# Optimization experiments

Measured on AMD Instinct MI355X. Metric: run time of the kernel, lower is better.

## Reference

```python
import jax, jax.numpy as jnp
import numpy as np

WS = 8            # window size (square)
NUM_HEADS = 8
DIM = 256
IMG = 256         # feature map H=W for mask construction
SHIFT = WS // 2
B = 4


def _rel_pos_index(Wh, Ww):
    coords = np.stack(np.meshgrid(np.arange(Wh), np.arange(Ww), indexing='ij'))  # (2,Wh,Ww)
    cf = coords.reshape(2, -1)
    rel = cf[:, :, None] - cf[:, None, :]        # (2,N,N)
    rel = rel.transpose(1, 2, 0).astype(np.int64)
    rel[..., 0] += Wh - 1
    rel[..., 1] += Ww - 1
    rel[..., 0] *= 2 * Ww - 1
    return rel.sum(-1)                           # (N,N)


def _shift_mask(H, W, ws, ss):
    # standard Swin shifted-window attention mask: (nW, ws*ws, ws*ws) with 0 / -100
    img = np.zeros((H, W), dtype=np.float32)
    cnt = 0
    for hs in (slice(0, -ws), slice(-ws, -ss), slice(-ss, None)):
        for wsl in (slice(0, -ws), slice(-ws, -ss), slice(-ss, None)):
            img[hs, wsl] = cnt
            cnt += 1
    m = img.reshape(H // ws, ws, W // ws, ws).transpose(0, 2, 1, 3).reshape(-1, ws * ws)
    am = m[:, None, :] - m[:, :, None]
    return np.where(am != 0, np.float32(-100.0), np.float32(0.0))


def setup_inputs() -> dict:
    key = jax.random.key(0)
    ks = jax.random.split(key, 10)
    nW = (IMG // WS) ** 2
    B_ = B * nW
    N = WS * WS
    x = jax.random.normal(ks[0], (B_, N, DIM), dtype=jnp.float32)
    y = jax.random.normal(ks[1], (B_, N, DIM), dtype=jnp.float32)
    mask = jnp.asarray(_shift_mask(IMG, IMG, WS, SHIFT))
    s = 0.02
    q_w = jax.random.normal(ks[2], (DIM, DIM), dtype=jnp.float32) * s
    q_b = jnp.zeros((DIM,), dtype=jnp.float32)
    kv_w = jax.random.normal(ks[3], (2 * DIM, DIM), dtype=jnp.float32) * s
    kv_b = jnp.zeros((2 * DIM,), dtype=jnp.float32)
    proj_w = jax.random.normal(ks[4], (DIM, DIM), dtype=jnp.float32) * s
    proj_b = jnp.zeros((DIM,), dtype=jnp.float32)
    rpb_table = jax.random.normal(ks[5], ((2 * WS - 1) ** 2, NUM_HEADS), dtype=jnp.float32) * s
    return {"x": x, "y": y, "mask": mask, "q_w": q_w, "q_b": q_b,
            "kv_w": kv_w, "kv_b": kv_b, "proj_w": proj_w, "proj_b": proj_b,
            "rpb_table": rpb_table}


def reference(x, y, mask, q_w, q_b, kv_w, kv_b, proj_w, proj_b, rpb_table):
    B_, N, C = x.shape
    H = NUM_HEADS
    hd = C // H
    scale = hd ** -0.5
    # projections
    q = (x @ q_w.T + q_b).reshape(B_, N, H, hd).transpose(0, 2, 1, 3) * scale  # (B_,H,N,hd)
    kv = (y @ kv_w.T + kv_b).reshape(B_, N, 2, H, hd)
    k = kv[:, :, 0].transpose(0, 2, 1, 3)  # (B_,H,N,hd)
    v = kv[:, :, 1].transpose(0, 2, 1, 3)
    attn = jnp.einsum('bhid,bhjd->bhij', q, k)  # (B_,H,N,N)
    # relative position bias gathered from table
    rpi = jnp.asarray(_rel_pos_index(WS, WS))           # (N,N) int
    bias = rpb_table[rpi.reshape(-1)].reshape(N, N, H).transpose(2, 0, 1)  # (H,N,N)
    attn = attn + bias[None]
    # shifted-window mask
    nW = mask.shape[0]
    attn = attn.reshape(B_ // nW, nW, H, N, N) + mask[None, :, None]
    attn = attn.reshape(B_, H, N, N)
    attn = jax.nn.softmax(attn, axis=-1)
    out = jnp.einsum('bhij,bhjd->bhid', attn, v)        # (B_,H,N,hd)
    out = out.transpose(0, 2, 1, 3).reshape(B_, N, C)
    return out @ proj_w.T + proj_b
```

## Files before the change

### kernel.cpp

```cpp
#include <hip/hip_runtime.h>

typedef _Float16 half_t;
typedef _Float16 half8  __attribute__((ext_vector_type(8)));
typedef _Float16 half4v __attribute__((ext_vector_type(4)));
typedef float    f32x4  __attribute__((ext_vector_type(4)));

#define ROWB   528
#define S_A    0
#define S_B    33792
#define S_Q    67584
#define S_K    101376
#define SMEM_BYTES 135168
#define SCALE  0.17677669529663687f

__global__ __launch_bounds__(256) void swin_prep(
    const float* __restrict__ q_w, const float* __restrict__ kv_w,
    const float* __restrict__ proj_w, const float* __restrict__ rpb,
    const float* __restrict__ mask,
    half_t* __restrict__ w16, half_t* __restrict__ fused)
{
    int t = blockIdx.x * 256 + threadIdx.x;
    if (t < 65536)        w16[t] = (half_t)(q_w[t] * SCALE);
    else if (t < 196608)  w16[t] = (half_t)kv_w[t - 65536];
    else if (t < 262144)  w16[t] = (half_t)proj_w[t - 196608];
    else if (t < 393216) {
        int u = t - 262144;
        int cls = u >> 15, rest = u & 32767;
        int h = rest >> 12, i = (rest >> 6) & 63, j = rest & 63;
        int idx = ((i >> 3) - (j >> 3) + 7) * 15 + ((i & 7) - (j & 7) + 7);
        int wsel = (cls == 0) ? 0 : (cls == 1) ? 31 : (cls == 2) ? 992 : 1023;
        fused[u] = (half_t)(rpb[idx * 8 + h] + mask[(size_t)wsel * 4096 + i * 64 + j]);
    }
}

static __device__ __forceinline__ unsigned pk2(float a, float b) {
    union { _Float16 h[2]; unsigned u; } t;
    t.h[0] = (_Float16)a; t.h[1] = (_Float16)b; return t.u;
}

__global__ __launch_bounds__(512, 2) void swin_main(
    const float* __restrict__ x, const float* __restrict__ y,
    const float* __restrict__ q_b, const float* __restrict__ kv_b,
    const float* __restrict__ proj_b,
    const half_t* __restrict__ w16, const half_t* __restrict__ fused,
    float* __restrict__ out)
{
    __shared__ __align__(16) char sm[SMEM_BYTES];
    const int tid  = threadIdx.x;
    const int w    = tid >> 6;
    const int lane = tid & 63;
    const int l15  = lane & 15;
    const int g    = lane >> 4;
    const int b    = blockIdx.x;
    const int jf0  = w * 32;

    const float* xb = x + (size_t)b * 16384;
    const float* yb = y + (size_t)b * 16384;

    {
        float4 fx[8], fy[8];
        #pragma unroll
        for (int it = 0; it < 4; ++it) {
            int c = tid + it * 512;
            int row = c >> 5, c8 = c & 31;
            fx[it*2+0] = *(const float4*)(xb + row * 256 + c8 * 8);
            fx[it*2+1] = *(const float4*)(xb + row * 256 + c8 * 8 + 4);
            fy[it*2+0] = *(const float4*)(yb + row * 256 + c8 * 8);
            fy[it*2+1] = *(const float4*)(yb + row * 256 + c8 * 8 + 4);
        }
        #pragma unroll
        for (int it = 0; it < 4; ++it) {
            int c = tid + it * 512;
            int row = c >> 5, c8 = c & 31;
            half8 hx, hy;
            #pragma unroll
            for (int e = 0; e < 4; ++e) {
                hx[e]   = (half_t)(&fx[it*2+0].x)[e];
                hx[e+4] = (half_t)(&fx[it*2+1].x)[e];
                hy[e]   = (half_t)(&fy[it*2+0].x)[e];
                hy[e+4] = (half_t)(&fy[it*2+1].x)[e];
            }
            int off = row * ROWB + c8 * 16;
            *(half8*)(sm + S_A + off) = hx;
            *(half8*)(sm + S_B + off) = hy;
        }
    }
    __syncthreads();

    unsigned vp[4][2][2];
    {
        const half_t* wkv = w16 + 65536;
        f32x4 ak[4][2], av[4][2];
        #pragma unroll
        for (int mt = 0; mt < 4; ++mt)
            #pragma unroll
            for (int nt = 0; nt < 2; ++nt) {
                f32x4 z = {0.f,0.f,0.f,0.f}; ak[mt][nt] = z; av[mt][nt] = z;
            }
        #pragma unroll
        for (int kh = 0; kh < 2; ++kh) {
            half8 wbk[4][2], wbv[4][2];
            #pragma unroll
            for (int k2 = 0; k2 < 4; ++k2) {
                int k0 = (kh * 4 + k2) * 32 + g * 8;
                #pragma unroll
                for (int nt = 0; nt < 2; ++nt) {
                    int jf = jf0 + nt * 16 + l15;
                    wbk[k2][nt] = *(const half8*)(wkv + jf * 256 + k0);
                    wbv[k2][nt] = *(const half8*)(wkv + (256 + jf) * 256 + k0);
                }
            }
            #pragma unroll
            for (int k2 = 0; k2 < 4; ++k2) {
                int k0 = (kh * 4 + k2) * 32 + g * 8;
                half8 a[4];
                #pragma unroll
                for (int mt = 0; mt < 4; ++mt)
                    a[mt] = *(const half8*)(sm + S_B + (mt * 16 + l15) * ROWB + k0 * 2);
                #pragma unroll
                for (int mt = 0; mt < 4; ++mt)
                    #pragma unroll
                    for (int nt = 0; nt < 2; ++nt) {
                        ak[mt][nt] = __builtin_amdgcn_mfma_f32_16x16x32_f16(a[mt], wbk[k2][nt], ak[mt][nt], 0, 0, 0);
                        av[mt][nt] = __builtin_amdgcn_mfma_f32_16x16x32_f16(a[mt], wbv[k2][nt], av[mt][nt], 0, 0, 0);
                    }
            }
        }
        #pragma unroll
        for (int nt = 0; nt < 2; ++nt) {
            int jf = jf0 + nt * 16 + l15;
            float kb = kv_b[jf];
            #pragma unroll
            for (int mt = 0; mt < 4; ++mt)
                #pragma unroll
                for (int r = 0; r < 4; ++r) {
                    int i = mt * 16 + g * 4 + r;
                    *(half_t*)(sm + S_K + i * ROWB + jf * 2) = (half_t)(ak[mt][nt][r] + kb);
                }
        }
        #pragma unroll
        for (int nt = 0; nt < 2; ++nt) {
            float vb = kv_b[256 + jf0 + nt * 16 + l15];
            #pragma unroll
            for (int mt = 0; mt < 4; ++mt) {
                vp[mt][nt][0] = pk2(av[mt][nt][0] + vb, av[mt][nt][1] + vb);
                vp[mt][nt][1] = pk2(av[mt][nt][2] + vb, av[mt][nt][3] + vb);
            }
        }
    }

    {
        const half_t* wq = w16;
        half8 wb[8][2];
        #pragma unroll
        for (int kc = 0; kc < 8; ++kc) {
            int k0 = kc * 32 + g * 8;
            #pragma unroll
            for (int nt = 0; nt < 2; ++nt)
                wb[kc][nt] = *(const half8*)(wq + (jf0 + nt * 16 + l15) * 256 + k0);
        }
        f32x4 acc[4][2];
        #pragma unroll
        for (int mt = 0; mt < 4; ++mt)
            #pragma unroll
            for (int nt = 0; nt < 2; ++nt) { f32x4 z = {0.f,0.f,0.f,0.f}; acc[mt][nt] = z; }
        #pragma unroll
        for (int kc = 0; kc < 8; ++kc) {
            int k0 = kc * 32 + g * 8;
            half8 a[4];
            #pragma unroll
            for (int mt = 0; mt < 4; ++mt)
                a[mt] = *(const half8*)(sm + S_A + (mt * 16 + l15) * ROWB + k0 * 2);
            #pragma unroll
            for (int mt = 0; mt < 4; ++mt)
                #pragma unroll
                for (int nt = 0; nt < 2; ++nt)
                    acc[mt][nt] = __builtin_amdgcn_mfma_f32_16x16x32_f16(a[mt], wb[kc][nt], acc[mt][nt], 0, 0, 0);
        }
        #pragma unroll
        for (int nt = 0; nt < 2; ++nt) {
            int jf = jf0 + nt * 16 + l15;
            float qbs = q_b[jf] * SCALE;
            #pragma unroll
            for (int mt = 0; mt < 4; ++mt)
                #pragma unroll
                for (int r = 0; r < 4; ++r) {
                    int i = mt * 16 + g * 4 + r;
                    *(half_t*)(sm + S_Q + i * ROWB + jf * 2) = (half_t)(acc[mt][nt][r] + qbs);
                }
        }
    }
    __syncthreads();

    {
        const int h = w;
        const int wi = b & 1023;
        const int cls = ((((wi >> 5) == 31) ? 2 : 0)) | (((wi & 31) == 31) ? 1 : 0);
        const half_t* fb = fused + ((size_t)cls * 8 + h) * 4096;
        const int k0 = jf0 + g * 8;

        half8 ka[4], qf[4];
        #pragma unroll
        for (int mt = 0; mt < 4; ++mt)
            ka[mt] = *(const half8*)(sm + S_K + (mt * 16 + l15) * ROWB + k0 * 2);
        #pragma unroll
        for (int nt = 0; nt < 4; ++nt)
            qf[nt] = *(const half8*)(sm + S_Q + (nt * 16 + l15) * ROWB + k0 * 2);
        half4v fm[4][4];
        #pragma unroll
        for (int nt = 0; nt < 4; ++nt)
            #pragma unroll
            for (int mt = 0; mt < 4; ++mt)
                fm[nt][mt] = *(const half4v*)(fb + (nt * 16 + l15) * 64 + mt * 16 + g * 4);

        f32x4 t[4][4];
        #pragma unroll
        for (int mt = 0; mt < 4; ++mt)
            #pragma unroll
            for (int nt = 0; nt < 4; ++nt) {
                f32x4 z = {0.f,0.f,0.f,0.f};
                t[mt][nt] = __builtin_amdgcn_mfma_f32_16x16x32_f16(ka[mt], qf[nt], z, 0, 0, 0);
            }

        #pragma unroll
        for (int nt = 0; nt < 4; ++nt) {
            #pragma unroll
            for (int mt = 0; mt < 4; ++mt)
                #pragma unroll
                for (int r = 0; r < 4; ++r)
                    t[mt][nt][r] += (float)fm[nt][mt][r];
            float m = -1e30f;
            #pragma unroll
            for (int mt = 0; mt < 4; ++mt)
                #pragma unroll
                for (int r = 0; r < 4; ++r) m = fmaxf(m, t[mt][nt][r]);
            m = fmaxf(m, __shfl_xor(m, 16));
            m = fmaxf(m, __shfl_xor(m, 32));
            float s = 0.f;
            #pragma unroll
            for (int mt = 0; mt < 4; ++mt)
                #pragma unroll
                for (int r = 0; r < 4; ++r) {
                    float p = __expf(t[mt][nt][r] - m);
                    t[mt][nt][r] = p;
                    s += p;
                }
            s += __shfl_xor(s, 16);
            s += __shfl_xor(s, 32);
            float inv = 1.f / s;
            #pragma unroll
            for (int mt = 0; mt < 4; ++mt)
                #pragma unroll
                for (int r = 0; r < 4; ++r) t[mt][nt][r] *= inv;
        }

        #pragma unroll
        for (int nt = 0; nt < 4; ++nt) {
            int i = nt * 16 + l15;
            #pragma unroll
            for (int mt = 0; mt < 4; ++mt) {
                int jc = (mt & 1) * 16 + g * 4;
                int base = (mt < 2) ? S_A : S_B;
                half4v pv;
                pv[0] = (half_t)t[mt][nt][0];
                pv[1] = (half_t)t[mt][nt][1];
                pv[2] = (half_t)t[mt][nt][2];
                pv[3] = (half_t)t[mt][nt][3];
                *(half4v*)(sm + base + i * ROWB + (jf0 + jc) * 2) = pv;
            }
        }

        half8 va[2][2];
        {
            int srcA = ((2 * g) & 3) * 16 + l15;
            int srcB = ((2 * g + 1) & 3) * 16 + l15;
            int hi = g >> 1;
            #pragma unroll
            for (int dt = 0; dt < 2; ++dt)
                #pragma unroll
                for (int kc = 0; kc < 2; ++kc) {
                    union { unsigned u[4]; half8 h; } u8;
                    #pragma unroll
                    for (int p = 0; p < 4; ++p) {
                        int src = (p >> 1) ? srcB : srcA;
                        unsigned rlo = __shfl(vp[kc * 2 + 0][dt][p & 1], src);
                        unsigned rhi = __shfl(vp[kc * 2 + 1][dt][p & 1], src);
                        u8.u[p] = hi ? rhi : rlo;
                    }
                    va[dt][kc] = u8.h;
                }
        }
        asm volatile("s_waitcnt lgkmcnt(0)" ::: "memory");
        __builtin_amdgcn_sched_barrier(0);

        f32x4 o[2][4];
        #pragma unroll
        for (int dt = 0; dt < 2; ++dt)
            #pragma unroll
            for (int nt = 0; nt < 4; ++nt) { f32x4 z = {0.f,0.f,0.f,0.f}; o[dt][nt] = z; }
        #pragma unroll
        for (int kc = 0; kc < 2; ++kc) {
            int jb = g * 8;
            int base = kc ? S_B : S_A;
            half8 pf[4];
            #pragma unroll
            for (int nt = 0; nt < 4; ++nt)
                pf[nt] = *(const half8*)(sm + base + (nt * 16 + l15) * ROWB + (jf0 + jb) * 2);
            #pragma unroll
            for (int dt = 0; dt < 2; ++dt)
                #pragma unroll
                for (int nt = 0; nt < 4; ++nt)
                    o[dt][nt] = __builtin_amdgcn_mfma_f32_16x16x32_f16(va[dt][kc], pf[nt], o[dt][nt], 0, 0, 0);
        }
        #pragma unroll
        for (int nt = 0; nt < 4; ++nt) {
            int i = nt * 16 + l15;
            #pragma unroll
            for (int dt = 0; dt < 2; ++dt) {
                int d0 = dt * 16 + g * 4;
                half4v ov;
                ov[0] = (half_t)o[dt][nt][0];
                ov[1] = (half_t)o[dt][nt][1];
                ov[2] = (half_t)o[dt][nt][2];
                ov[3] = (half_t)o[dt][nt][3];
                *(half4v*)(sm + S_A + i * ROWB + (jf0 + d0) * 2) = ov;
            }
        }
    }
    __syncthreads();

    {
        const half_t* wp = w16 + 196608;
        half8 wb[8][2];
        #pragma unroll
        for (int kc = 0; kc < 8; ++kc) {
            int k0 = kc * 32 + g * 8;
            #pragma unroll
            for (int nt = 0; nt < 2; ++nt)
                wb[kc][nt] = *(const half8*)(wp + (jf0 + nt * 16 + l15) * 256 + k0);
        }
        f32x4 acc[4][2];
        #pragma unroll
        for (int mt = 0; mt < 4; ++mt)
            #pragma unroll
            for (int nt = 0; nt < 2; ++nt) { f32x4 z = {0.f,0.f,0.f,0.f}; acc[mt][nt] = z; }
        #pragma unroll
        for (int kc = 0; kc < 8; ++kc) {
            int k0 = kc * 32 + g * 8;
            half8 a[4];
            #pragma unroll
            for (int mt = 0; mt < 4; ++mt)
                a[mt] = *(const half8*)(sm + S_A + (mt * 16 + l15) * ROWB + k0 * 2);
            #pragma unroll
            for (int mt = 0; mt < 4; ++mt)
                #pragma unroll
                for (int nt = 0; nt < 2; ++nt)
                    acc[mt][nt] = __builtin_amdgcn_mfma_f32_16x16x32_f16(a[mt], wb[kc][nt], acc[mt][nt], 0, 0, 0);
        }
        float* ob = out + (size_t)b * 16384;
        #pragma unroll
        for (int nt = 0; nt < 2; ++nt) {
            int jf = jf0 + nt * 16 + l15;
            float pbv = proj_b[jf];
            #pragma unroll
            for (int mt = 0; mt < 4; ++mt)
                #pragma unroll
                for (int r = 0; r < 4; ++r) {
                    int i = mt * 16 + g * 4 + r;
                    ob[i * 256 + jf] = acc[mt][nt][r] + pbv;
                }
        }
    }
}

extern "C" void kernel_launch(void* const* d_in, const int* in_sizes, int n_in,
                              void* d_out, int out_size, void* d_ws, size_t ws_size,
                              hipStream_t stream) {
    const float* x      = (const float*)d_in[0];
    const float* y      = (const float*)d_in[1];
    const float* mask   = (const float*)d_in[2];
    const float* q_w    = (const float*)d_in[3];
    const float* q_b    = (const float*)d_in[4];
    const float* kv_w   = (const float*)d_in[5];
    const float* kv_b   = (const float*)d_in[6];
    const float* proj_w = (const float*)d_in[7];
    const float* proj_b = (const float*)d_in[8];
    const float* rpb    = (const float*)d_in[9];

    half_t* w16   = (half_t*)d_ws;
    half_t* fused = (half_t*)((char*)d_ws + 524288);

    swin_prep<<<1536, 256, 0, stream>>>(q_w, kv_w, proj_w, rpb, mask, w16, fused);
    swin_main<<<4096, 512, 0, stream>>>(x, y, q_b, kv_b, proj_b,
                                        w16, fused, (float*)d_out);
}
```

Before: 444.8 us.

## Keep Q/K/P fragments in registers via shuffles, halve LDS, raise occupancy

Computes the Q and K projections transposed, so each wave already holds its head's features in its MFMA output layout. Operand fragments for QK^T, and P and V for PV, are then built with cross-lane shuffles instead of round-tripping through LDS. This removes the Q/K shared buffers and halves LDS to 66 KB, and launch bounds are raised to 4 blocks per CU. Several block-wide barriers and LDS write/read passes go away, at the cost of extra shuffle instructions and tighter register limits that risk spills.

Measured after the change: 518.1 us. 16.5% more time.

```diff
diff --git a/kernel.cpp b/kernel.cpp
--- a/kernel.cpp
+++ b/kernel.cpp
@@ -8,9 +8,7 @@
 #define ROWB   528
 #define S_A    0
 #define S_B    33792
-#define S_Q    67584
-#define S_K    101376
-#define SMEM_BYTES 135168
+#define SMEM_BYTES 67584
 #define SCALE  0.17677669529663687f
 
 __global__ __launch_bounds__(256) void swin_prep(
@@ -38,7 +36,20 @@
     t.h[0] = (_Float16)a; t.h[1] = (_Float16)b; return t.u;
 }
 
-__global__ __launch_bounds__(512, 2) void swin_main(
+#define BUILD_FRAG(dst, P0, P1)                                          \
+    do {                                                                 \
+        union { unsigned u[4]; half8 h; } _u;                            \
+        _Pragma("unroll")                                                \
+        for (int p = 0; p < 4; ++p) {                                    \
+            int _src = (p >> 1) ? srcB : srcA;                           \
+            unsigned _rlo = (unsigned)__shfl((int)(P0)[p & 1], _src);    \
+            unsigned _rhi = (unsigned)__shfl((int)(P1)[p & 1], _src);    \
+            _u.u[p] = hi ? _rhi : _rlo;                                  \
+        }                                                                \
+        dst = _u.h;                                                      \
+    } while (0)
+
+__global__ __launch_bounds__(512, 4) void swin_main(
     const float* __restrict__ x, const float* __restrict__ y,
     const float* __restrict__ q_b, const float* __restrict__ kv_b,
     const float* __restrict__ proj_b,
@@ -53,9 +64,13 @@
     const int g    = lane >> 4;
     const int b    = blockIdx.x;
     const int jf0  = w * 32;
+    const int srcA = ((2 * g) & 3) * 16 + l15;
+    const int srcB = ((2 * g + 1) & 3) * 16 + l15;
+    const int hi   = g >> 1;
 
     const float* xb = x + (size_t)b * 16384;
     const float* yb = y + (size_t)b * 16384;
+    const half_t* wkv = w16 + 65536;
 
     {
         float4 fx[8], fy[8];
@@ -87,131 +102,125 @@
     }
     __syncthreads();
 
-    unsigned vp[4][2][2];
+    f32x4 kacc[2][4], vacc[4][2];
+    #pragma unroll
+    for (int ft = 0; ft < 2; ++ft)
+        #pragma unroll
+        for (int tok = 0; tok < 4; ++tok) {
+            f32x4 z = {0.f,0.f,0.f,0.f}; kacc[ft][tok] = z; vacc[tok][ft] = z;
+        }
+    #pragma unroll
+    for (int kh = 0; kh < 2; ++kh) {
+        half8 wbk[4][2], wbv[4][2];
+        #pragma unroll
+        for (int k2 = 0; k2 < 4; ++k2) {
+            int k0 = (kh * 4 + k2) * 32 + g * 8;
+            #pragma unroll
+            for (int ft = 0; ft < 2; ++ft) {
+                int jf = jf0 + ft * 16 + l15;
+                wbk[k2][ft] = *(const half8*)(wkv + jf * 256 + k0);
+                wbv[k2][ft] = *(const half8*)(wkv + (256 + jf) * 256 + k0);
+            }
+        }
+        #pragma unroll
+        for (int k2 = 0; k2 < 4; ++k2) {
+            int k0 = (kh * 4 + k2) * 32 + g * 8;
+            half8 a[4];
+            #pragma unroll
+            for (int tok = 0; tok < 4; ++tok)
+                a[tok] = *(const half8*)(sm + S_B + (tok * 16 + l15) * ROWB + k0 * 2);
+            #pragma unroll
+            for (int ft = 0; ft < 2; ++ft)
+                #pragma unroll
+                for (int tok = 0; tok < 4; ++tok) {
+                    kacc[ft][tok] = __builtin_amdgcn_mfma_f32_16x16x32_f16(wbk[k2][ft], a[tok], kacc[ft][tok], 0, 0, 0);
+                    vacc[tok][ft] = __builtin_amdgcn_mfma_f32_16x16x32_f16(a[tok], wbv[k2][ft], vacc[tok][ft], 0, 0, 0);
+                }
+        }
+    }
+    __syncthreads();
+
+    unsigned kp[2][4][2], vp[4][2][2];
     {
-        const half_t* wkv = w16 + 65536;
-        f32x4 ak[4][2], av[4][2];
-        #pragma unroll
-        for (int mt = 0; mt < 4; ++mt)
-            #pragma unroll
-            for (int nt = 0; nt < 2; ++nt) {
-                f32x4 z = {0.f,0.f,0.f,0.f}; ak[mt][nt] = z; av[mt][nt] = z;
-            }
+        #pragma unroll
+        for (int ft = 0; ft < 2; ++ft) {
+            float4 kb4 = *(const float4*)(kv_b + jf0 + ft * 16 + g * 4);
+            #pragma unroll
+            for (int tok = 0; tok < 4; ++tok) {
+                kp[ft][tok][0] = pk2(kacc[ft][tok][0] + kb4.x, kacc[ft][tok][1] + kb4.y);
+                kp[ft][tok][1] = pk2(kacc[ft][tok][2] + kb4.z, kacc[ft][tok][3] + kb4.w);
+            }
+        }
+        #pragma unroll
+        for (int ft = 0; ft < 2; ++ft) {
+            float vb = kv_b[256 + jf0 + ft * 16 + l15];
+            #pragma unroll
+            for (int tok = 0; tok < 4; ++tok) {
+                vp[tok][ft][0] = pk2(vacc[tok][ft][0] + vb, vacc[tok][ft][1] + vb);
+                vp[tok][ft][1] = pk2(vacc[tok][ft][2] + vb, vacc[tok][ft][3] + vb);
+            }
+        }
+    }
+
+    unsigned qp[2][4][2];
+    {
+        f32x4 qacc[2][4];
+        #pragma unroll
+        for (int ft = 0; ft < 2; ++ft)
+            #pragma unroll
+            for (int tok = 0; tok < 4; ++tok) { f32x4 z = {0.f,0.f,0.f,0.f}; qacc[ft][tok] = z; }
         #pragma unroll
         for (int kh = 0; kh < 2; ++kh) {
-            half8 wbk[4][2], wbv[4][2];
+            half8 wbq[4][2];
             #pragma unroll
             for (int k2 = 0; k2 < 4; ++k2) {
                 int k0 = (kh * 4 + k2) * 32 + g * 8;
                 #pragma unroll
-                for (int nt = 0; nt < 2; ++nt) {
-                    int jf = jf0 + nt * 16 + l15;
-                    wbk[k2][nt] = *(const half8*)(wkv + jf * 256 + k0);
-                    wbv[k2][nt] = *(const half8*)(wkv + (256 + jf) * 256 + k0);
-                }
+                for (int ft = 0; ft < 2; ++ft)
+                    wbq[k2][ft] = *(const half8*)(w16 + (jf0 + ft * 16 + l15) * 256 + k0);
             }
             #pragma unroll
             for (int k2 = 0; k2 < 4; ++k2) {
                 int k0 = (kh * 4 + k2) * 32 + g * 8;
                 half8 a[4];
                 #pragma unroll
-                for (int mt = 0; mt < 4; ++mt)
-                    a[mt] = *(const half8*)(sm + S_B + (mt * 16 + l15) * ROWB + k0 * 2);
-                #pragma unroll
-                for (int mt = 0; mt < 4; ++mt)
+                for (int tok = 0; tok < 4; ++tok)
+                    a[tok] = *(const half8*)(sm + S_A + (tok * 16 + l15) * ROWB + k0 * 2);
+                #pragma unroll
+                for (int ft = 0; ft < 2; ++ft)
                     #pragma unroll
-                    for (int nt = 0; nt < 2; ++nt) {
-                        ak[mt][nt] = __builtin_amdgcn_mfma_f32_16x16x32_f16(a[mt], wbk[k2][nt], ak[mt][nt], 0, 0, 0);
-                        av[mt][nt] = __builtin_amdgcn_mfma_f32_16x16x32_f16(a[mt], wbv[k2][nt], av[mt][nt], 0, 0, 0);
-                    }
-            }
-        }
-        #pragma unroll
-        for (int nt = 0; nt < 2; ++nt) {
-            int jf = jf0 + nt * 16 + l15;
-            float kb = kv_b[jf];
-            #pragma unroll
-            for (int mt = 0; mt < 4; ++mt)
-                #pragma unroll
-                for (int r = 0; r < 4; ++r) {
-                    int i = mt * 16 + g * 4 + r;
-                    *(half_t*)(sm + S_K + i * ROWB + jf * 2) = (half_t)(ak[mt][nt][r] + kb);
-                }
-        }
-        #pragma unroll
-        for (int nt = 0; nt < 2; ++nt) {
-            float vb = kv_b[256 + jf0 + nt * 16 + l15];
-            #pragma unroll
-            for (int mt = 0; mt < 4; ++mt) {
-                vp[mt][nt][0] = pk2(av[mt][nt][0] + vb, av[mt][nt][1] + vb);
-                vp[mt][nt][1] = pk2(av[mt][nt][2] + vb, av[mt][nt][3] + vb);
+                    for (int tok = 0; tok < 4; ++tok)
+                        qacc[ft][tok] = __builtin_amdgcn_mfma_f32_16x16x32_f16(wbq[k2][ft], a[tok], qacc[ft][tok], 0, 0, 0);
+            }
+        }
+        #pragma unroll
+        for (int ft = 0; ft < 2; ++ft) {
+            float4 qb4 = *(const float4*)(q_b + jf0 + ft * 16 + g * 4);
+            #pragma unroll
+            for (int tok = 0; tok < 4; ++tok) {
+                qp[ft][tok][0] = pk2(qacc[ft][tok][0] + qb4.x * SCALE, qacc[ft][tok][1] + qb4.y * SCALE);
+                qp[ft][tok][1] = pk2(qacc[ft][tok][2] + qb4.z * SCALE, qacc[ft][tok][3] + qb4.w * SCALE);
             }
         }
     }
 
     {
-        const half_t* wq = w16;
-        half8 wb[8][2];
-        #pragma unroll
-        for (int kc = 0; kc < 8; ++kc) {
-            int k0 = kc * 32 + g * 8;
-            #pragma unroll
-            for (int nt = 0; nt < 2; ++nt)
-                wb[kc][nt] = *(const half8*)(wq + (jf0 + nt * 16 + l15) * 256 + k0);
-        }
-        f32x4 acc[4][2];
-        #pragma unroll
-        for (int mt = 0; mt < 4; ++mt)
-            #pragma unroll
-            for (int nt = 0; nt < 2; ++nt) { f32x4 z = {0.f,0.f,0.f,0.f}; acc[mt][nt] = z; }
-        #pragma unroll
-        for (int kc = 0; kc < 8; ++kc) {
-            int k0 = kc * 32 + g * 8;
-            half8 a[4];
-            #pragma unroll
-            for (int mt = 0; mt < 4; ++mt)
-                a[mt] = *(const half8*)(sm + S_A + (mt * 16 + l15) * ROWB + k0 * 2);
-            #pragma unroll
-            for (int mt = 0; mt < 4; ++mt)
-                #pragma unroll
-                for (int nt = 0; nt < 2; ++nt)
-                    acc[mt][nt] = __builtin_amdgcn_mfma_f32_16x16x32_f16(a[mt], wb[kc][nt], acc[mt][nt], 0, 0, 0);
-        }
-        #pragma unroll
-        for (int nt = 0; nt < 2; ++nt) {
-            int jf = jf0 + nt * 16 + l15;
-            float qbs = q_b[jf] * SCALE;
-            #pragma unroll
-            for (int mt = 0; mt < 4; ++mt)
-                #pragma unroll
-                for (int r = 0; r < 4; ++r) {
-                    int i = mt * 16 + g * 4 + r;
-                    *(half_t*)(sm + S_Q + i * ROWB + jf * 2) = (half_t)(acc[mt][nt][r] + qbs);
-                }
-        }
-    }
-    __syncthreads();
-
-    {
-        const int h = w;
         const int wi = b & 1023;
         const int cls = ((((wi >> 5) == 31) ? 2 : 0)) | (((wi & 31) == 31) ? 1 : 0);
-        const half_t* fb = fused + ((size_t)cls * 8 + h) * 4096;
-        const int k0 = jf0 + g * 8;
+        const half_t* fb = fused + ((size_t)cls * 8 + w) * 4096;
+
+        half4v fm[4][4];
+        #pragma unroll
+        for (int nt = 0; nt < 4; ++nt)
+            #pragma unroll
+            for (int mt = 0; mt < 4; ++mt)
+                fm[nt][mt] = *(const half4v*)(fb + (nt * 16 + l15) * 64 + mt * 16 + g * 4);
 
         half8 ka[4], qf[4];
         #pragma unroll
-        for (int mt = 0; mt < 4; ++mt)
-            ka[mt] = *(const half8*)(sm + S_K + (mt * 16 + l15) * ROWB + k0 * 2);
-        #pragma unroll
-        for (int nt = 0; nt < 4; ++nt)
-            qf[nt] = *(const half8*)(sm + S_Q + (nt * 16 + l15) * ROWB + k0 * 2);
-        half4v fm[4][4];
-        #pragma unroll
-        for (int nt = 0; nt < 4; ++nt)
-            #pragma unroll
-            for (int mt = 0; mt < 4; ++mt)
-                fm[nt][mt] = *(const half4v*)(fb + (nt * 16 + l15) * 64 + mt * 16 + g * 4);
+        for (int mt = 0; mt < 4; ++mt) BUILD_FRAG(ka[mt], kp[0][mt], kp[1][mt]);
+        #pragma unroll
+        for (int nt = 0; nt < 4; ++nt) BUILD_FRAG(qf[nt], qp[0][nt], qp[1][nt]);
 
         f32x4 t[4][4];
         #pragma unroll
@@ -254,120 +263,87 @@
                 for (int r = 0; r < 4; ++r) t[mt][nt][r] *= inv;
         }
 
+        unsigned pp[4][4][2];
+        #pragma unroll
+        for (int mt = 0; mt < 4; ++mt)
+            #pragma unroll
+            for (int nt = 0; nt < 4; ++nt) {
+                pp[mt][nt][0] = pk2(t[mt][nt][0], t[mt][nt][1]);
+                pp[mt][nt][1] = pk2(t[mt][nt][2], t[mt][nt][3]);
+            }
+
+        f32x4 o[2][4];
+        #pragma unroll
+        for (int dt = 0; dt < 2; ++dt)
+            #pragma unroll
+            for (int nt = 0; nt < 4; ++nt) { f32x4 z = {0.f,0.f,0.f,0.f}; o[dt][nt] = z; }
+        #pragma unroll
+        for (int kc = 0; kc < 2; ++kc) {
+            half8 va[2], pf[4];
+            #pragma unroll
+            for (int dt = 0; dt < 2; ++dt) BUILD_FRAG(va[dt], vp[kc*2+0][dt], vp[kc*2+1][dt]);
+            #pragma unroll
+            for (int nt = 0; nt < 4; ++nt) BUILD_FRAG(pf[nt], pp[kc*2+0][nt], pp[kc*2+1][nt]);
+            #pragma unroll
+            for (int dt = 0; dt < 2; ++dt)
+                #pragma unroll
+                for (int nt = 0; nt < 4; ++nt)
+                    o[dt][nt] = __builtin_amdgcn_mfma_f32_16x16x32_f16(va[dt], pf[nt], o[dt][nt], 0, 0, 0);
+        }
+
+        half8 wbp[8][2];
+        #pragma unroll
+        for (int kc = 0; kc < 8; ++kc) {
+            int k0 = kc * 32 + g * 8;
+            #pragma unroll
+            for (int ft = 0; ft < 2; ++ft)
+                wbp[kc][ft] = *(const half8*)(w16 + 196608 + (jf0 + ft * 16 + l15) * 256 + k0);
+        }
+
         #pragma unroll
         for (int nt = 0; nt < 4; ++nt) {
             int i = nt * 16 + l15;
             #pragma unroll
-            for (int mt = 0; mt < 4; ++mt) {
-                int jc = (mt & 1) * 16 + g * 4;
-                int base = (mt < 2) ? S_A : S_B;
-                half4v pv;
-                pv[0] = (half_t)t[mt][nt][0];
-                pv[1] = (half_t)t[mt][nt][1];
-                pv[2] = (half_t)t[mt][nt][2];
-                pv[3] = (half_t)t[mt][nt][3];
-                *(half4v*)(sm + base + i * ROWB + (jf0 + jc) * 2) = pv;
-            }
-        }
-
-        half8 va[2][2];
-        {
-            int srcA = ((2 * g) & 3) * 16 + l15;
-            int srcB = ((2 * g + 1) & 3) * 16 + l15;
-            int hi = g >> 1;
-            #pragma unroll
-            for (int dt = 0; dt < 2; ++dt)
-                #pragma unroll
-                for (int kc = 0; kc < 2; ++kc) {
-                    union { unsigned u[4]; half8 h; } u8;
-                    #pragma unroll
-                    for (int p = 0; p < 4; ++p) {
-                        int src = (p >> 1) ? srcB : srcA;
-                        unsigned rlo = __shfl(vp[kc * 2 + 0][dt][p & 1], src);
-                        unsigned rhi = __shfl(vp[kc * 2 + 1][dt][p & 1], src);
-                        u8.u[p] = hi ? rhi : rlo;
-                    }
-                    va[dt][kc] = u8.h;
-                }
-        }
-        asm volatile("s_waitcnt lgkmcnt(0)" ::: "memory");
-        __builtin_amdgcn_sched_barrier(0);
-
-        f32x4 o[2][4];
-        #pragma unroll
-        for (int dt = 0; dt < 2; ++dt)
-            #pragma unroll
-            for (int nt = 0; nt < 4; ++nt) { f32x4 z = {0.f,0.f,0.f,0.f}; o[dt][nt] = z; }
-        #pragma unroll
-        for (int kc = 0; kc < 2; ++kc) {
-            int jb = g * 8;
-            int base = kc ? S_B : S_A;
-            half8 pf[4];
-            #pragma unroll
-            for (int nt = 0; nt < 4; ++nt)
-                pf[nt] = *(const half8*)(sm + base + (nt * 16 + l15) * ROWB + (jf0 + jb) * 2);
-            #pragma unroll
-            for (int dt = 0; dt < 2; ++dt)
-                #pragma unroll
-                for (int nt = 0; nt < 4; ++nt)
-                    o[dt][nt] = __builtin_amdgcn_mfma_f32_16x16x32_f16(va[dt][kc], pf[nt], o[dt][nt], 0, 0, 0);
-        }
-        #pragma unroll
-        for (int nt = 0; nt < 4; ++nt) {
-            int i = nt * 16 + l15;
-            #pragma unroll
             for (int dt = 0; dt < 2; ++dt) {
-                int d0 = dt * 16 + g * 4;
                 half4v ov;
                 ov[0] = (half_t)o[dt][nt][0];
                 ov[1] = (half_t)o[dt][nt][1];
                 ov[2] = (half_t)o[dt][nt][2];
                 ov[3] = (half_t)o[dt][nt][3];
-                *(half4v*)(sm + S_A + i * ROWB + (jf0 + d0) * 2) = ov;
-            }
-        }
-    }
-    __syncthreads();
-
-    {
-        const half_t* wp = w16 + 196608;
-        half8 wb[8][2];
-        #pragma unroll
-        for (int kc = 0; kc < 8; ++kc) {
-            int k0 = kc * 32 + g * 8;
-            #pragma unroll
-            for (int nt = 0; nt < 2; ++nt)
-                wb[kc][nt] = *(const half8*)(wp + (jf0 + nt * 16 + l15) * 256 + k0);
-        }
+                *(half4v*)(sm + S_B + i * ROWB + (jf0 + dt * 16 + g * 4) * 2) = ov;
+            }
+        }
+        __syncthreads();
+
         f32x4 acc[4][2];
         #pragma unroll
         for (int mt = 0; mt < 4; ++mt)
             #pragma unroll
-            for (int nt = 0; nt < 2; ++nt) { f32x4 z = {0.f,0.f,0.f,0.f}; acc[mt][nt] = z; }
+            for (int ft = 0; ft < 2; ++ft) { f32x4 z = {0.f,0.f,0.f,0.f}; acc[mt][ft] = z; }
         #pragma unroll
         for (int kc = 0; kc < 8; ++kc) {
             int k0 = kc * 32 + g * 8;
             half8 a[4];
             #pragma unroll
             for (int mt = 0; mt < 4; ++mt)
-                a[mt] = *(const half8*)(sm + S_A + (mt * 16 + l15) * ROWB + k0 * 2);
-            #pragma unroll
-            for (int mt = 0; mt < 4; ++mt)
-                #pragma unroll
-                for (int nt = 0; nt < 2; ++nt)
-                    acc[mt][nt] = __builtin_amdgcn_mfma_f32_16x16x32_f16(a[mt], wb[kc][nt], acc[mt][nt], 0, 0, 0);
+                a[mt] = *(const half8*)(sm + S_B + (mt * 16 + l15) * ROWB + k0 * 2);
+            #pragma unroll
+            for (int mt = 0; mt < 4; ++mt)
+                #pragma unroll
+                for (int ft = 0; ft < 2; ++ft)
+                    acc[mt][ft] = __builtin_amdgcn_mfma_f32_16x16x32_f16(a[mt], wbp[kc][ft], acc[mt][ft], 0, 0, 0);
         }
         float* ob = out + (size_t)b * 16384;
         #pragma unroll
-        for (int nt = 0; nt < 2; ++nt) {
-            int jf = jf0 + nt * 16 + l15;
+        for (int ft = 0; ft < 2; ++ft) {
+            int jf = jf0 + ft * 16 + l15;
             float pbv = proj_b[jf];
             #pragma unroll
             for (int mt = 0; mt < 4; ++mt)
                 #pragma unroll
                 for (int r = 0; r < 4; ++r) {
                     int i = mt * 16 + g * 4 + r;
-                    ob[i * 256 + jf] = acc[mt][nt][r] + pbv;
+                    ob[i * 256 + jf] = acc[mt][ft][r] + pbv;
                 }
         }
     }
```
